# Optimization experiments

Hardware: AMD Instinct MI355X
Metric: run time of the kernel (lower is better)

Reference implementation:

```python
import jax, jax.numpy as jnp
import numpy as np

D = 256; NH = 8; NL = 4; NP = 4; DH = D // NH; FF = 1024; B = 2
SHAPES = np.array([[112, 112], [56, 56], [28, 28], [14, 14]], np.int32)  # (H_l, W_l)
SIZES = (SHAPES[:, 0] * SHAPES[:, 1]).astype(np.int64)
STARTS = np.concatenate([[0], np.cumsum(SIZES)])
S = int(SIZES.sum())


def setup_inputs() -> dict:
    key = jax.random.key(0)
    ks = jax.random.split(key, 10)
    def w(k, shape, s=0.02):
        return (s * jax.random.normal(k, shape)).astype(jnp.float32)
    z = lambda *sh: jnp.zeros(sh, jnp.float32)
    return dict(
        src=w(ks[0], (B, S, D), 1.0),
        pos=w(ks[1], (B, S, D), 1.0),
        reference_points=jax.random.uniform(ks[2], (B, S, NL, 2), jnp.float32),
        spatial_shapes=jnp.asarray(SHAPES),
        level_start_index=jnp.asarray(STARTS[:-1].astype(np.int32)),
        W_off=w(ks[3], (D, NH * NL * NP * 2)), b_off=z(NH * NL * NP * 2),
        W_attn=w(ks[4], (D, NH * NL * NP)), b_attn=z(NH * NL * NP),
        W_val=w(ks[5], (D, D)), b_val=z(D),
        W_out=w(ks[6], (D, D)), b_out=z(D),
        g1=jnp.ones((D,), jnp.float32), be1=z(D),
        g2=jnp.ones((D,), jnp.float32), be2=z(D),
        W1=w(ks[7], (D, FF)), b1=z(FF),
        W2=w(ks[8], (FF, D)), b2=z(D),
    )


def _ln(x, g, b):
    m = x.mean(-1, keepdims=True)
    v = ((x - m) ** 2).mean(-1, keepdims=True)
    return (x - m) * jax.lax.rsqrt(v + 1e-5) * g + b


def _bilinear(value, Hl, Wl, loc):
    # value: [B, NH, Hl*Wl, DH]; loc: [B, S, NH, NP, 2] in [0,1] (x,y)
    # grid_sample semantics: align_corners=False, padding_mode='zeros'
    b, s = loc.shape[0], loc.shape[1]
    x = loc[..., 0] * Wl - 0.5
    y = loc[..., 1] * Hl - 0.5
    x0 = jnp.floor(x); y0 = jnp.floor(y)
    dx = x - x0; dy = y - y0
    out = jnp.zeros((b, s, NH, NP, DH), value.dtype)
    corners = ((x0, y0, (1 - dx) * (1 - dy)), (x0 + 1, y0, dx * (1 - dy)),
               (x0, y0 + 1, (1 - dx) * dy), (x0 + 1, y0 + 1, dx * dy))
    for cx, cy, wgt in corners:
        valid = (cx >= 0) & (cx < Wl) & (cy >= 0) & (cy < Hl)
        idx = (jnp.clip(cy, 0, Hl - 1) * Wl + jnp.clip(cx, 0, Wl - 1)).astype(jnp.int32)
        idx = idx.transpose(0, 2, 1, 3).reshape(b, NH, s * NP)  # [B,NH,S*NP]
        v = jnp.take_along_axis(value, idx[..., None], axis=2)   # [B,NH,S*NP,DH]
        v = v.reshape(b, NH, s, NP, DH).transpose(0, 2, 1, 3, 4)  # [B,S,NH,NP,DH]
        out = out + v * (wgt * valid.astype(value.dtype))[..., None]
    return out


def _msda(query, src, ref, W_off, b_off, W_attn, b_attn, W_val, b_val, W_out, b_out):
    b, s, _ = query.shape
    value = src @ W_val + b_val                                   # [B,S,D]
    off = (query @ W_off + b_off).reshape(b, s, NH, NL, NP, 2)
    aw = jax.nn.softmax((query @ W_attn + b_attn).reshape(b, s, NH, NL * NP), axis=-1)
    aw = aw.reshape(b, s, NH, NL, NP)
    wh = jnp.asarray(SHAPES[:, ::-1].astype(np.float32))          # [L,2] as (W,H)
    loc = ref[:, :, None, :, None, :] + off / wh[None, None, None, :, None, :]
    out = jnp.zeros((b, s, NH, DH), value.dtype)
    for l in range(NL):
        Hl, Wl = int(SHAPES[l, 0]), int(SHAPES[l, 1])
        v_l = value[:, STARTS[l]:STARTS[l + 1]].reshape(b, Hl * Wl, NH, DH)
        v_l = v_l.transpose(0, 2, 1, 3)                           # [B,NH,HW,DH]
        samp = _bilinear(v_l, Hl, Wl, loc[:, :, :, l])            # [B,S,NH,NP,DH]
        out = out + jnp.einsum('bshp,bshpd->bshd', aw[:, :, :, l], samp)
    return out.reshape(b, s, D) @ W_out + b_out


def reference(src, pos, reference_points, spatial_shapes, level_start_index,
              W_off, b_off, W_attn, b_attn, W_val, b_val, W_out, b_out,
              g1, be1, g2, be2, W1, b1, W2, b2):
    q = src + pos
    src2 = _msda(q, src, reference_points, W_off, b_off, W_attn, b_attn,
                 W_val, b_val, W_out, b_out)
    x = _ln(src + src2, g1, be1)
    f = jnp.maximum(x @ W1 + b1, 0.0) @ W2 + b2
    return _ln(x + f, g2, be2)
```

## Files before the change

### kernel.cpp

```cpp
#include <hip/hip_runtime.h>

constexpr int D_   = 256;
constexpr int NH_  = 8;
constexpr int DH_  = 32;
constexpr int NL_  = 4;
constexpr int NP_  = 4;
constexpr int FF_  = 1024;
constexpr int B_   = 2;
constexpr int S_   = 16660;
constexpr int NR_  = B_ * S_;

typedef __attribute__((ext_vector_type(8))) short bf16x8;
typedef __attribute__((ext_vector_type(4))) float f32x4;

__device__ __forceinline__ ushort f2bf(float f) {
  unsigned u = __float_as_uint(f);
  return (ushort)((u + 0x7FFFu + ((u >> 16) & 1u)) >> 16);
}

__global__ __launch_bounds__(256)
void prep_kernel(const float* __restrict__ src, const float* __restrict__ pos,
                 ushort* __restrict__ qb, ushort* __restrict__ srcb, int n4) {
  int i = blockIdx.x * 256 + threadIdx.x;
  if (i >= n4) return;
  float4 s = ((const float4*)src)[i];
  float4 p = ((const float4*)pos)[i];
  ushort4 sb = {f2bf(s.x), f2bf(s.y), f2bf(s.z), f2bf(s.w)};
  ushort4 q  = {f2bf(s.x + p.x), f2bf(s.y + p.y), f2bf(s.z + p.z), f2bf(s.w + p.w)};
  ((ushort4*)srcb)[i] = sb;
  ((ushort4*)qb)[i]   = q;
}

__global__ __launch_bounds__(256)
void cvt_weights(const float* __restrict__ Woff, const float* __restrict__ Wattn,
                 const float* __restrict__ Wval, const float* __restrict__ Wout,
                 const float* __restrict__ W1,  const float* __restrict__ W2,
                 ushort* __restrict__ out) {
  const int wi = blockIdx.y;
  const int i = blockIdx.x * 256 + threadIdx.x;
  const float* src; int K, N; size_t off;
  switch (wi) {
    case 0: src = Wval;  K = 256;  N = 256;  off = 0;      break;
    case 1: src = Woff;  K = 256;  N = 256;  off = 65536;  break;
    case 2: src = Wattn; K = 256;  N = 128;  off = 131072; break;
    case 3: src = Wout;  K = 256;  N = 256;  off = 163840; break;
    case 4: src = W1;    K = 256;  N = 1024; off = 229376; break;
    default:src = W2;    K = 1024; N = 256;  off = 491520; break;
  }
  if (i >= K * N) return;
  int k = i / N, n = i - k * N;
  out[off + (size_t)n * K + k] = f2bf(src[i]);
}

template<int MODE>
__global__ __launch_bounds__(256, 2)
void gemm_blds(const ushort* __restrict__ A, const ushort* __restrict__ Wpan,
               const float* __restrict__ bias, const float* __restrict__ bias2,
               void* __restrict__ C, void* __restrict__ C2, int M, int Ns) {
  __shared__ ushort Bs[128 * 256];
  const int tid = threadIdx.x;
  const int l = tid & 63, w = tid >> 6;
  const int l15 = l & 15, kg = l >> 4;
  const int cxor = l15 & 7;
  const int bx = blockIdx.x, by = blockIdx.y;

  const int r0 = bx * 128 + w * 16 + l15;
  const int r1 = r0 + 64;
  const int r0c = min(r0, M - 1), r1c = min(r1, M - 1);
  const ushort* a0p = A + (size_t)r0c * 256 + kg * 8;
  const ushort* a1p = A + (size_t)r1c * 256 + kg * 8;
  bf16x8 a0[8], a1[8];
#pragma unroll
  for (int kk = 0; kk < 8; ++kk) a0[kk] = *(const bf16x8*)(a0p + kk * 32);
#pragma unroll
  for (int kk = 0; kk < 8; ++kk) a1[kk] = *(const bf16x8*)(a1p + kk * 32);

  const ushort* wp = Wpan + (size_t)by * 128 * 256;
#pragma unroll
  for (int rnd = 0; rnd < 16; ++rnd) {
    int gi = rnd * 256 + tid;
    int col = gi >> 5;
    int gphys = gi & 31;
    int glog = gphys ^ (col & 7);
    __builtin_amdgcn_global_load_lds(
        (const __attribute__((address_space(1))) void*)(wp + (size_t)col * 256 + glog * 8),
        (__attribute__((address_space(3))) void*)(Bs + (size_t)(rnd * 256 + w * 64) * 8),
        16, 0, 0);
  }

  float bj[8];
#pragma unroll
  for (int ct = 0; ct < 8; ++ct) {
    int colg = by * 128 + ct * 16 + l15;
    if (MODE == 3) bj[ct] = (colg < 256) ? bias[colg] : bias2[colg - 256];
    else           bj[ct] = bias[colg];
  }

  __syncthreads();

  f32x4 acc0[8], acc1[8];
#pragma unroll
  for (int ct = 0; ct < 8; ++ct) {
    acc0[ct] = (f32x4){0.f, 0.f, 0.f, 0.f};
    acc1[ct] = (f32x4){0.f, 0.f, 0.f, 0.f};
  }
#pragma unroll
  for (int ct = 0; ct < 8; ++ct) {
    const int cb = (ct * 16 + l15) * 256;
#pragma unroll
    for (int kk = 0; kk < 8; ++kk) {
      bf16x8 b = *(const bf16x8*)(Bs + cb + (((kk * 4 + kg) ^ cxor) * 8));
      acc0[ct] = __builtin_amdgcn_mfma_f32_16x16x32_bf16(a0[kk], b, acc0[ct], 0, 0, 0);
      acc1[ct] = __builtin_amdgcn_mfma_f32_16x16x32_bf16(a1[kk], b, acc1[ct], 0, 0, 0);
    }
  }

  const int orow0 = bx * 128 + w * 16 + kg * 4;
#pragma unroll
  for (int sl = 0; sl < 2; ++sl) {
    const int rowb = orow0 + sl * 64;
#pragma unroll
    for (int ct = 0; ct < 8; ++ct) {
      const int colg = by * 128 + ct * 16 + l15;
#pragma unroll
      for (int r = 0; r < 4; ++r) {
        const int row = rowb + r;
        if (row >= M) continue;
        float v = (sl ? acc1[ct][r] : acc0[ct][r]) + bj[ct];
        if (MODE == 2) v = fmaxf(v, 0.f);
        if (MODE == 3) {
          if (colg < 256) ((float*)C )[(size_t)row * 256 + colg]       = v;
          else            ((float*)C2)[(size_t)row * 128 + (colg-256)] = v;
        } else if (MODE == 0) {
          ((float*)C)[(size_t)row * Ns + colg] = v;
        } else {
          ((ushort*)C)[(size_t)row * Ns + colg] = f2bf(v);
        }
      }
    }
  }
}

template<bool RELU, bool OUTBF16>
__global__ __launch_bounds__(256, 2)
void gemm_mfma(const ushort* __restrict__ A, const ushort* __restrict__ Wt,
               const float* __restrict__ bias, void* __restrict__ Cout,
               int M, int N, int K) {
  __shared__ ushort As[128 * 32];
  __shared__ ushort Bs[128 * 32];
  const int tid = threadIdx.x;
  const int l = tid & 63, w = tid >> 6;
  const int brow = blockIdx.x * 128, bcol = blockIdx.y * 128;

  const int rA0 = w * 32 + (l >> 2);
  const int kbl = (l & 3) ^ ((rA0 >> 1) & 3);
  const ushort* agp0 = A  + (size_t)(brow + rA0)      * K + kbl * 8;
  const ushort* agp1 = A  + (size_t)(brow + rA0 + 16) * K + kbl * 8;
  const ushort* bgp0 = Wt + (size_t)(bcol + rA0)      * K + kbl * 8;
  const ushort* bgp1 = Wt + (size_t)(bcol + rA0 + 16) * K + kbl * 8;
  ushort* asl0 = As + w * 1024; ushort* asl1 = asl0 + 512;
  ushort* bsl0 = Bs + w * 1024; ushort* bsl1 = bsl0 + 512;

  const int l15 = l & 15;
  const int kg  = l >> 4;
  const int swz = (l15 >> 1) & 3;
  const int rbase = (w & 1) * 64, cbase = (w >> 1) * 64;
  const int aoff = (rbase + l15) * 32 + ((kg ^ swz) * 8);
  const int boff = (cbase + l15) * 32 + ((kg ^ swz) * 8);

  f32x4 acc[4][4];
#pragma unroll
  for (int i = 0; i < 4; ++i)
#pragma unroll
    for (int j = 0; j < 4; ++j) acc[i][j] = (f32x4){0.f, 0.f, 0.f, 0.f};

  for (int bk = 0; bk < K; bk += 32) {
    __builtin_amdgcn_global_load_lds(
        (const __attribute__((address_space(1))) void*)(agp0 + bk),
        (__attribute__((address_space(3))) void*)asl0, 16, 0, 0);
    __builtin_amdgcn_global_load_lds(
        (const __attribute__((address_space(1))) void*)(agp1 + bk),
        (__attribute__((address_space(3))) void*)asl1, 16, 0, 0);
    __builtin_amdgcn_global_load_lds(
        (const __attribute__((address_space(1))) void*)(bgp0 + bk),
        (__attribute__((address_space(3))) void*)bsl0, 16, 0, 0);
    __builtin_amdgcn_global_load_lds(
        (const __attribute__((address_space(1))) void*)(bgp1 + bk),
        (__attribute__((address_space(3))) void*)bsl1, 16, 0, 0);
    __syncthreads();

    bf16x8 af[4], bfr[4];
#pragma unroll
    for (int i = 0; i < 4; ++i) af[i]  = *(const bf16x8*)(As + aoff + i * 512);
#pragma unroll
    for (int j = 0; j < 4; ++j) bfr[j] = *(const bf16x8*)(Bs + boff + j * 512);
#pragma unroll
    for (int i = 0; i < 4; ++i)
#pragma unroll
      for (int j = 0; j < 4; ++j)
        acc[i][j] = __builtin_amdgcn_mfma_f32_16x16x32_bf16(af[i], bfr[j], acc[i][j], 0, 0, 0);
    __syncthreads();
  }

  const int r0 = kg * 4;
#pragma unroll
  for (int j = 0; j < 4; ++j) {
    const int col = bcol + cbase + j * 16 + l15;
    const float bj = bias[col];
#pragma unroll
    for (int i = 0; i < 4; ++i) {
      const int rowb = brow + rbase + i * 16 + r0;
#pragma unroll
      for (int r = 0; r < 4; ++r) {
        const int row = rowb + r;
        if (row < M) {
          float v = acc[i][j][r] + bj;
          if (RELU) v = fmaxf(v, 0.f);
          if (OUTBF16) ((ushort*)Cout)[(size_t)row * N + col] = f2bf(v);
          else         ((float*)Cout)[(size_t)row * N + col]  = v;
        }
      }
    }
  }
}

__global__ __launch_bounds__(256)
void msda_kernel(const ushort* __restrict__ value, const float* __restrict__ offs,
                 const float* __restrict__ attn, const float* __restrict__ ref,
                 ushort* __restrict__ out) {
  __shared__ int4   descI[4 * 136];
  __shared__ float4 descW[4 * 136];
  const int t = threadIdx.x;
  const int orig = blockIdx.x;
  const int xcd = orig & 7, ii = orig >> 3;
  const int wg = (xcd < 2 ? xcd * 1042 : 2 * 1042 + (xcd - 2) * 1041) + ii;
  const int n0 = wg * 4;

  const int Hs[4] = {112, 56, 28, 14};
  const int st[4] = {0, 12544, 15680, 16464};

#pragma unroll
  for (int rep = 0; rep < 2; ++rep) {
    const int di = t + rep * 256;
    const int q = di >> 7, h = (di >> 4) & 7, lp = di & 15;
    const int lv = lp >> 2;
    const int n = n0 + q;

    float lg = attn[(size_t)n * 128 + h * 16 + lp];
    float mx = lg;
#pragma unroll
    for (int o = 8; o; o >>= 1) mx = fmaxf(mx, __shfl_xor(mx, o, 64));
    float e = __expf(lg - mx);
    float ssum = e;
#pragma unroll
    for (int o = 8; o; o >>= 1) ssum += __shfl_xor(ssum, o, 64);
    const float aw = e / ssum;

    const int Hl = Hs[lv], Wl = Hs[lv];
    const float fS = (float)Wl;
    const float refx = ref[((size_t)n * 4 + lv) * 2 + 0];
    const float refy = ref[((size_t)n * 4 + lv) * 2 + 1];
    const float ox = offs[(size_t)n * 256 + h * 32 + lp * 2 + 0];
    const float oy = offs[(size_t)n * 256 + h * 32 + lp * 2 + 1];
    float x = fmaf(refx, fS, ox) - 0.5f;
    float y = fmaf(refy, fS, oy) - 0.5f;
    float x0f = floorf(x), y0f = floorf(y);
    float dx = x - x0f, dy = y - y0f;
    int x0 = (int)x0f, y0 = (int)y0f;
    int x0c = min(max(x0, 0), Wl - 1), x1c = min(max(x0 + 1, 0), Wl - 1);
    int y0c = min(max(y0, 0), Hl - 1), y1c = min(max(y0 + 1, 0), Hl - 1);
    bool vx0 = (x0 >= 0) && (x0 < Wl), vx1 = (x0 + 1 >= 0) && (x0 + 1 < Wl);
    bool vy0 = (y0 >= 0) && (y0 < Hl), vy1 = (y0 + 1 >= 0) && (y0 + 1 < Hl);
    int4 I;
    I.x = st[lv] + y0c * Wl + x0c;
    I.y = st[lv] + y0c * Wl + x1c;
    I.z = st[lv] + y1c * Wl + x0c;
    I.w = st[lv] + y1c * Wl + x1c;
    float4 Wv;
    Wv.x = (1.f - dx) * (1.f - dy) * ((vx0 && vy0) ? aw : 0.f);
    Wv.y = dx * (1.f - dy)         * ((vx1 && vy0) ? aw : 0.f);
    Wv.z = (1.f - dx) * dy         * ((vx0 && vy1) ? aw : 0.f);
    Wv.w = dx * dy                 * ((vx1 && vy1) ? aw : 0.f);
    const int slot = q * 136 + h * 17 + lp;
    descI[slot] = I;
    descW[slot] = Wv;
  }
  __syncthreads();

  const int q = t >> 6, lane = t & 63;
  const int h = lane >> 3, c = lane & 7;
  const int n = n0 + q;
  const int b = n / S_;
  const ushort* base = value + (size_t)b * S_ * 256 + h * 32 + c * 4;

  float a0 = 0.f, a1 = 0.f, a2 = 0.f, a3 = 0.f;
#pragma unroll
  for (int pt = 0; pt < 16; ++pt) {
    const int slot = q * 136 + h * 17 + pt;
    int4 I = descI[slot];
    float4 Wv = descW[slot];
    int   Ia[4] = {I.x, I.y, I.z, I.w};
    float Wa[4] = {Wv.x, Wv.y, Wv.z, Wv.w};
#pragma unroll
    for (int cr = 0; cr < 4; ++cr) {
      uint2 u = *(const uint2*)(base + (size_t)Ia[cr] * 256);
      float f0 = __uint_as_float(u.x << 16);
      float f1 = __uint_as_float(u.x & 0xffff0000u);
      float f2 = __uint_as_float(u.y << 16);
      float f3 = __uint_as_float(u.y & 0xffff0000u);
      a0 = fmaf(Wa[cr], f0, a0);
      a1 = fmaf(Wa[cr], f1, a1);
      a2 = fmaf(Wa[cr], f2, a2);
      a3 = fmaf(Wa[cr], f3, a3);
    }
  }
  ushort4 o = {f2bf(a0), f2bf(a1), f2bf(a2), f2bf(a3)};
  *(ushort4*)(out + (size_t)n * 256 + h * 32 + c * 4) = o;
}

template<bool WB>
__global__ __launch_bounds__(256)
void add_ln_kernel(const float* __restrict__ a, const float* __restrict__ r,
                   const float* __restrict__ g, const float* __restrict__ be,
                   float* __restrict__ out, ushort* __restrict__ outb, int M) {
  const int wave = threadIdx.x >> 6;
  const int lane = threadIdx.x & 63;
  const int row = blockIdx.x * 4 + wave;
  if (row >= M) return;
  const float4 av = *(const float4*)(a + (size_t)row * 256 + lane * 4);
  const float4 rv = *(const float4*)(r + (size_t)row * 256 + lane * 4);
  float4 v = {av.x + rv.x, av.y + rv.y, av.z + rv.z, av.w + rv.w};
  float s  = v.x + v.y + v.z + v.w;
  float s2 = v.x * v.x + v.y * v.y + v.z * v.z + v.w * v.w;
#pragma unroll
  for (int o = 32; o > 0; o >>= 1) {
    s  += __shfl_xor(s, o, 64);
    s2 += __shfl_xor(s2, o, 64);
  }
  const float mean = s * (1.f / 256.f);
  const float var  = s2 * (1.f / 256.f) - mean * mean;
  const float rstd = rsqrtf(var + 1e-5f);
  const float4 gv = *(const float4*)(g + lane * 4);
  const float4 bv = *(const float4*)(be + lane * 4);
  float4 o4;
  o4.x = (v.x - mean) * rstd * gv.x + bv.x;
  o4.y = (v.y - mean) * rstd * gv.y + bv.y;
  o4.z = (v.z - mean) * rstd * gv.z + bv.z;
  o4.w = (v.w - mean) * rstd * gv.w + bv.w;
  *(float4*)(out + (size_t)row * 256 + lane * 4) = o4;
  if (WB) {
    ushort4 ob = {f2bf(o4.x), f2bf(o4.y), f2bf(o4.z), f2bf(o4.w)};
    ((ushort4*)(outb + (size_t)row * 256))[lane] = ob;
  }
}

extern "C" void kernel_launch(void* const* d_in, const int* in_sizes, int n_in,
                              void* d_out, int out_size, void* d_ws, size_t ws_size,
                              hipStream_t stream) {
  const float* src    = (const float*)d_in[0];
  const float* pos    = (const float*)d_in[1];
  const float* refpts = (const float*)d_in[2];
  const float* W_off  = (const float*)d_in[5];
  const float* b_off  = (const float*)d_in[6];
  const float* W_attn = (const float*)d_in[7];
  const float* b_attn = (const float*)d_in[8];
  const float* W_val  = (const float*)d_in[9];
  const float* b_val  = (const float*)d_in[10];
  const float* W_out  = (const float*)d_in[11];
  const float* b_out  = (const float*)d_in[12];
  const float* g1     = (const float*)d_in[13];
  const float* be1    = (const float*)d_in[14];
  const float* g2     = (const float*)d_in[15];
  const float* be2    = (const float*)d_in[16];
  const float* W1     = (const float*)d_in[17];
  const float* b1     = (const float*)d_in[18];
  const float* W2     = (const float*)d_in[19];
  const float* b2     = (const float*)d_in[20];
  float* out = (float*)d_out;

  const size_t NF = (size_t)NR_ * 256;
  char* p = (char*)d_ws;
  ushort* qb   = (ushort*)p; p += NF * 2;
  ushort* srcb = (ushort*)p; p += NF * 2;
  ushort* valb = (ushort*)p; p += NF * 2;
  float*  offs = (float*) p; p += NF * 4;
  float*  attn = (float*) p; p += NF * 2;
  float*  tmp  = (float*) p; p += NF * 4;
  float*  x    = (float*) p; p += NF * 4;
  ushort* Wt   = (ushort*)p; p += 753664 * 2;
  ushort* msdab = srcb;
  ushort* xb    = qb;
  ushort* hid   = valb;
  ushort* WtVal = Wt;
  ushort* WtOA  = Wt + 65536;
  ushort* WtOut = Wt + 163840;
  ushort* Wt1   = Wt + 229376;
  ushort* Wt2   = Wt + 491520;

  dim3 blk(256);
  const int n4 = NR_ * 64;
  const int gr = (NR_ + 127) / 128;

  prep_kernel<<<(n4 + 255) / 256, blk, 0, stream>>>(src, pos, qb, srcb, n4);
  cvt_weights<<<dim3(1024, 6), blk, 0, stream>>>(W_off, W_attn, W_val, W_out, W1, W2, Wt);
  gemm_blds<1><<<dim3(gr, 2), blk, 0, stream>>>(srcb, WtVal, b_val, nullptr,
                                                valb, nullptr, NR_, 256);
  gemm_blds<3><<<dim3(gr, 3), blk, 0, stream>>>(qb, WtOA, b_off, b_attn,
                                                offs, attn, NR_, 0);
  msda_kernel<<<NR_ / 4, blk, 0, stream>>>(valb, offs, attn, refpts, msdab);
  gemm_blds<0><<<dim3(gr, 2), blk, 0, stream>>>(msdab, WtOut, b_out, nullptr,
                                                tmp, nullptr, NR_, 256);
  add_ln_kernel<true ><<<(NR_ + 3) / 4, blk, 0, stream>>>(tmp, src, g1, be1, x, xb, NR_);
  gemm_blds<2><<<dim3(gr, 8), blk, 0, stream>>>(xb, Wt1, b1, nullptr,
                                                hid, nullptr, NR_, 1024);
  gemm_mfma<false, false><<<dim3(gr, 2), blk, 0, stream>>>(hid, Wt2, b2, tmp, NR_, 256, 1024);
  add_ln_kernel<false><<<(NR_ + 3) / 4, blk, 0, stream>>>(tmp, x, g2, be2, out, nullptr, NR_);
}
```

Before: 410.6 us.

## Add panel-LDS GEMM for FFN down-projection and widen MSDA gather loads

Replaces the generic K-loop GEMM for the FF2 projection with a kernel that stages a 128x256 weight panel in swizzled LDS per chunk and keeps the A fragments in registers read straight from global memory. This cuts the barrier count per K step and raises MFMA work per sync. Separately, the MSDA sampling kernel now loads 8 bf16 channels per lane with 128-bit reads, splits the sampling points across two half-waves, and combines them with a cross-lane shuffle, so each gather request moves more data. The trade-offs are 64KB of LDS per block in the new GEMM, which may cap occupancy, and more registers per lane in the sampling kernel.

```diff
diff --git a/kernel.cpp b/kernel.cpp
--- a/kernel.cpp
+++ b/kernel.cpp
@@ -141,6 +141,85 @@
   }
 }
 
+__global__ __launch_bounds__(256, 2)
+void gemm_blds1024(const ushort* __restrict__ A, const ushort* __restrict__ Wpan,
+                   const float* __restrict__ bias, float* __restrict__ C, int M) {
+  __shared__ ushort Bs[128 * 256];
+  const int tid = threadIdx.x;
+  const int l = tid & 63, w = tid >> 6;
+  const int l15 = l & 15, kg = l >> 4;
+  const int cxor = l15 & 7;
+  const int bx = blockIdx.x, by = blockIdx.y;
+
+  const int r0 = bx * 128 + w * 16 + l15;
+  const int r1 = r0 + 64;
+  const int r0c = min(r0, M - 1), r1c = min(r1, M - 1);
+  const ushort* a0p = A + (size_t)r0c * 1024 + kg * 8;
+  const ushort* a1p = A + (size_t)r1c * 1024 + kg * 8;
+  const ushort* wp = Wpan + (size_t)by * 128 * 1024;
+
+  float bj[8];
+#pragma unroll
+  for (int ct = 0; ct < 8; ++ct) bj[ct] = bias[by * 128 + ct * 16 + l15];
+
+  f32x4 acc0[8], acc1[8];
+#pragma unroll
+  for (int ct = 0; ct < 8; ++ct) {
+    acc0[ct] = (f32x4){0.f, 0.f, 0.f, 0.f};
+    acc1[ct] = (f32x4){0.f, 0.f, 0.f, 0.f};
+  }
+
+  for (int kc = 0; kc < 4; ++kc) {
+#pragma unroll
+    for (int rnd = 0; rnd < 16; ++rnd) {
+      int gi = rnd * 256 + tid;
+      int col = gi >> 5;
+      int gphys = gi & 31;
+      int glog = gphys ^ (col & 7);
+      __builtin_amdgcn_global_load_lds(
+          (const __attribute__((address_space(1))) void*)
+              (wp + (size_t)col * 1024 + kc * 256 + glog * 8),
+          (__attribute__((address_space(3))) void*)(Bs + (size_t)(rnd * 256 + w * 64) * 8),
+          16, 0, 0);
+    }
+    bf16x8 a0[8], a1[8];
+#pragma unroll
+    for (int kk = 0; kk < 8; ++kk) a0[kk] = *(const bf16x8*)(a0p + kc * 256 + kk * 32);
+#pragma unroll
+    for (int kk = 0; kk < 8; ++kk) a1[kk] = *(const bf16x8*)(a1p + kc * 256 + kk * 32);
+
+    __syncthreads();
+
+#pragma unroll
+    for (int ct = 0; ct < 8; ++ct) {
+      const int cb = (ct * 16 + l15) * 256;
+#pragma unroll
+      for (int kk = 0; kk < 8; ++kk) {
+        bf16x8 b = *(const bf16x8*)(Bs + cb + (((kk * 4 + kg) ^ cxor) * 8));
+        acc0[ct] = __builtin_amdgcn_mfma_f32_16x16x32_bf16(a0[kk], b, acc0[ct], 0, 0, 0);
+        acc1[ct] = __builtin_amdgcn_mfma_f32_16x16x32_bf16(a1[kk], b, acc1[ct], 0, 0, 0);
+      }
+    }
+    __syncthreads();
+  }
+
+  const int orow0 = bx * 128 + w * 16 + kg * 4;
+#pragma unroll
+  for (int sl = 0; sl < 2; ++sl) {
+    const int rowb = orow0 + sl * 64;
+#pragma unroll
+    for (int ct = 0; ct < 8; ++ct) {
+      const int colg = by * 128 + ct * 16 + l15;
+#pragma unroll
+      for (int r = 0; r < 4; ++r) {
+        const int row = rowb + r;
+        if (row >= M) continue;
+        C[(size_t)row * 256 + colg] = (sl ? acc1[ct][r] : acc0[ct][r]) + bj[ct];
+      }
+    }
+  }
+}
+
 template<bool RELU, bool OUTBF16>
 __global__ __launch_bounds__(256, 2)
 void gemm_mfma(const ushort* __restrict__ A, const ushort* __restrict__ Wt,
@@ -151,7 +230,6 @@
   const int tid = threadIdx.x;
   const int l = tid & 63, w = tid >> 6;
   const int brow = blockIdx.x * 128, bcol = blockIdx.y * 128;
-
   const int rA0 = w * 32 + (l >> 2);
   const int kbl = (l & 3) ^ ((rA0 >> 1) & 3);
   const ushort* agp0 = A  + (size_t)(brow + rA0)      * K + kbl * 8;
@@ -160,20 +238,17 @@
   const ushort* bgp1 = Wt + (size_t)(bcol + rA0 + 16) * K + kbl * 8;
   ushort* asl0 = As + w * 1024; ushort* asl1 = asl0 + 512;
   ushort* bsl0 = Bs + w * 1024; ushort* bsl1 = bsl0 + 512;
-
   const int l15 = l & 15;
   const int kg  = l >> 4;
   const int swz = (l15 >> 1) & 3;
   const int rbase = (w & 1) * 64, cbase = (w >> 1) * 64;
   const int aoff = (rbase + l15) * 32 + ((kg ^ swz) * 8);
   const int boff = (cbase + l15) * 32 + ((kg ^ swz) * 8);
-
   f32x4 acc[4][4];
 #pragma unroll
   for (int i = 0; i < 4; ++i)
 #pragma unroll
     for (int j = 0; j < 4; ++j) acc[i][j] = (f32x4){0.f, 0.f, 0.f, 0.f};
-
   for (int bk = 0; bk < K; bk += 32) {
     __builtin_amdgcn_global_load_lds(
         (const __attribute__((address_space(1))) void*)(agp0 + bk),
@@ -188,7 +263,6 @@
         (const __attribute__((address_space(1))) void*)(bgp1 + bk),
         (__attribute__((address_space(3))) void*)bsl1, 16, 0, 0);
     __syncthreads();
-
     bf16x8 af[4], bfr[4];
 #pragma unroll
     for (int i = 0; i < 4; ++i) af[i]  = *(const bf16x8*)(As + aoff + i * 512);
@@ -201,7 +275,6 @@
         acc[i][j] = __builtin_amdgcn_mfma_f32_16x16x32_bf16(af[i], bfr[j], acc[i][j], 0, 0, 0);
     __syncthreads();
   }
-
   const int r0 = kg * 4;
 #pragma unroll
   for (int j = 0; j < 4; ++j) {
@@ -288,14 +361,17 @@
   __syncthreads();
 
   const int q = t >> 6, lane = t & 63;
-  const int h = lane >> 3, c = lane & 7;
+  const int pth = lane >> 5;
+  const int h  = (lane >> 2) & 7;
+  const int cq = lane & 3;
   const int n = n0 + q;
   const int b = n / S_;
-  const ushort* base = value + (size_t)b * S_ * 256 + h * 32 + c * 4;
-
-  float a0 = 0.f, a1 = 0.f, a2 = 0.f, a3 = 0.f;
-#pragma unroll
-  for (int pt = 0; pt < 16; ++pt) {
+  const ushort* base = value + (size_t)b * S_ * 256 + h * 32 + cq * 8;
+
+  float a[8] = {0.f, 0.f, 0.f, 0.f, 0.f, 0.f, 0.f, 0.f};
+#pragma unroll
+  for (int pt2 = 0; pt2 < 8; ++pt2) {
+    const int pt = pt2 * 2 + pth;
     const int slot = q * 136 + h * 17 + pt;
     int4 I = descI[slot];
     float4 Wv = descW[slot];
@@ -303,19 +379,28 @@
     float Wa[4] = {Wv.x, Wv.y, Wv.z, Wv.w};
 #pragma unroll
     for (int cr = 0; cr < 4; ++cr) {
-      uint2 u = *(const uint2*)(base + (size_t)Ia[cr] * 256);
-      float f0 = __uint_as_float(u.x << 16);
-      float f1 = __uint_as_float(u.x & 0xffff0000u);
-      float f2 = __uint_as_float(u.y << 16);
-      float f3 = __uint_as_float(u.y & 0xffff0000u);
-      a0 = fmaf(Wa[cr], f0, a0);
-      a1 = fmaf(Wa[cr], f1, a1);
-      a2 = fmaf(Wa[cr], f2, a2);
-      a3 = fmaf(Wa[cr], f3, a3);
-    }
-  }
-  ushort4 o = {f2bf(a0), f2bf(a1), f2bf(a2), f2bf(a3)};
-  *(ushort4*)(out + (size_t)n * 256 + h * 32 + c * 4) = o;
+      uint4 u = *(const uint4*)(base + (size_t)Ia[cr] * 256);
+      const float wgt = Wa[cr];
+      a[0] = fmaf(wgt, __uint_as_float(u.x << 16),         a[0]);
+      a[1] = fmaf(wgt, __uint_as_float(u.x & 0xffff0000u), a[1]);
+      a[2] = fmaf(wgt, __uint_as_float(u.y << 16),         a[2]);
+      a[3] = fmaf(wgt, __uint_as_float(u.y & 0xffff0000u), a[3]);
+      a[4] = fmaf(wgt, __uint_as_float(u.z << 16),         a[4]);
+      a[5] = fmaf(wgt, __uint_as_float(u.z & 0xffff0000u), a[5]);
+      a[6] = fmaf(wgt, __uint_as_float(u.w << 16),         a[6]);
+      a[7] = fmaf(wgt, __uint_as_float(u.w & 0xffff0000u), a[7]);
+    }
+  }
+#pragma unroll
+  for (int i = 0; i < 8; ++i) a[i] += __shfl_xor(a[i], 32, 64);
+  if (pth == 0) {
+    uint4 o;
+    o.x = ((uint)f2bf(a[1]) << 16) | f2bf(a[0]);
+    o.y = ((uint)f2bf(a[3]) << 16) | f2bf(a[2]);
+    o.z = ((uint)f2bf(a[5]) << 16) | f2bf(a[4]);
+    o.w = ((uint)f2bf(a[7]) << 16) | f2bf(a[6]);
+    *(uint4*)(out + (size_t)n * 256 + h * 32 + cq * 8) = o;
+  }
 }
 
 template<bool WB>
@@ -413,6 +498,6 @@
   add_ln_kernel<true ><<<(NR_ + 3) / 4, blk, 0, stream>>>(tmp, src, g1, be1, x, xb, NR_);
   gemm_blds<2><<<dim3(gr, 8), blk, 0, stream>>>(xb, Wt1, b1, nullptr,
                                                 hid, nullptr, NR_, 1024);
-  gemm_mfma<false, false><<<dim3(gr, 2), blk, 0, stream>>>(hid, Wt2, b2, tmp, NR_, 256, 1024);
+  gemm_blds1024<<<dim3(gr, 2), blk, 0, stream>>>(hid, Wt2, b2, tmp, NR_);
   add_ln_kernel<false><<<(NR_ + 3) / 4, blk, 0, stream>>>(tmp, x, g2, be2, out, nullptr, NR_);
 }
```

Result: faster. 396.7 us (-3.4%).
